# Optimization experiments

Measured on AMD Instinct MI355X. Metric: run time of the kernel, lower is better.

## Reference

```python
import jax, jax.numpy as jnp
import numpy as np

C = 128  # in_channels

def setup_inputs() -> dict:
    key = jax.random.key(0)
    k1, k2, k3, k4 = jax.random.split(key, 4)
    b, c, h, w = 4, C, 64, 64
    feature0 = jax.random.normal(k1, (b, c, h, w), dtype=jnp.float32)
    flow = jax.random.normal(k2, (b, 2, h, w), dtype=jnp.float32)
    # Linear weights stored torch-style as [out, in]; xavier-uniform-like scale
    lim = float(np.sqrt(6.0 / (c + c)))
    Wq = jax.random.uniform(k3, (c, c), minval=-lim, maxval=lim, dtype=jnp.float32)
    Wk = jax.random.uniform(k4, (c, c), minval=-lim, maxval=lim, dtype=jnp.float32)
    bq = jnp.zeros((c,), dtype=jnp.float32)
    bk = jnp.zeros((c,), dtype=jnp.float32)
    return {"feature0": feature0, "flow": flow, "Wq": Wq, "bq": bq, "Wk": Wk, "bk": bk}

def reference(feature0, flow, Wq, bq, Wk, bk):
    b, c, h, w = feature0.shape
    n = h * w
    # [b, n, c]
    x = feature0.reshape(b, c, n).transpose(0, 2, 1)
    query = x @ Wq.T + bq                     # q_proj(feature0)
    key = query @ Wk.T + bk                   # NOTE: k_proj applied to query (as in source)
    value = flow.reshape(b, flow.shape[1], n).transpose(0, 2, 1)  # [b, n, 2]
    scores = jnp.einsum('bnc,bmc->bnm', query, key) / jnp.sqrt(jnp.float32(c))
    prob = jax.nn.softmax(scores, axis=-1)    # [b, n, n]
    out = jnp.einsum('bnm,bmv->bnv', prob, value)  # [b, n, 2]
    return out.reshape(b, h, w, value.shape[-1]).transpose(0, 3, 1, 2)
```

## Files before the change

kernel.cpp:

```cpp
#include <hip/hip_runtime.h>
#include <hip/hip_bf16.h>

constexpr int CH = 128;
constexpr int NPOS = 4096;
constexpr int NB = 4;
constexpr int SPLITS = 8;

typedef __bf16 bf16x8 __attribute__((ext_vector_type(8)));
typedef float f32x2 __attribute__((ext_vector_type(2)));
typedef float f32x16 __attribute__((ext_vector_type(16)));

constexpr float CSC = 0.08838834764831845f * 1.4426950408889634f;


__device__ __forceinline__ void async_copy16(const void* g, void* l) {
  auto gp = (const __attribute__((address_space(1))) unsigned int*)((uintptr_t)g);
  auto lp = (__attribute__((address_space(3))) unsigned int*)((uintptr_t)l);
  __builtin_amdgcn_global_load_lds(gp, lp, 16, 0, 0);
}

#define PIPE_BARRIER(N)                                              \
  asm volatile("s_waitcnt vmcnt(" #N ") lgkmcnt(0)\n\ts_barrier" ::: "memory")

__global__ __launch_bounds__(128) void fuse_w_kernel(
    const float* __restrict__ Wq, const float* __restrict__ bq,
    const float* __restrict__ Wk, const float* __restrict__ bk,
    __bf16* __restrict__ Wqb, __bf16* __restrict__ Wqkb,
    float* __restrict__ bqk) {
  __shared__ float red[CH];
  const int o = blockIdx.x;
  const int i = threadIdx.x;
  float acc = 0.f;
#pragma unroll 8
  for (int m = 0; m < CH; m++) acc += Wk[o * CH + m] * Wq[m * CH + i];
  Wqkb[o * CH + i] = (__bf16)acc;
  Wqb[o * CH + i] = (__bf16)Wq[o * CH + i];
  red[i] = Wk[o * CH + i] * bq[i];
  __syncthreads();
  if (i == 0) {
    float s = 0.f;
    for (int m = 0; m < CH; m++) s += red[m];
    bqk[o] = s + bk[o];
  }
}

__global__ __launch_bounds__(64) void proj_kernel(
    const float* __restrict__ feature0, const __bf16* __restrict__ Wqb,
    const float* __restrict__ bq, const __bf16* __restrict__ Wqkb,
    const float* __restrict__ bqk, __bf16* __restrict__ Qf,
    __bf16* __restrict__ Kf) {
  const int bid = blockIdx.x;
  const int b = (bid >> 1) & 3;
  const int u = (bid >> 3) * 2 + (bid & 1);
  const int lane = threadIdx.x;
  const int half = lane >> 5, l31 = lane & 31;
  const int pos = u * 32 + l31;

  bf16x8 A[8];
#pragma unroll
  for (int ks = 0; ks < 8; ks++) {
    float v[8];
#pragma unroll
    for (int j = 0; j < 8; j++)
      v[j] = feature0[(size_t)(b * CH + ks * 16 + half * 8 + j) * NPOS + pos];
#pragma unroll
    for (int j = 0; j < 8; j++) A[ks][j] = (__bf16)v[j];
  }

#pragma unroll
  for (int z = 0; z < 2; z++) {
    const __bf16* W = z ? Wqkb : Wqb;
    const float* bias = z ? bqk : bq;
    __bf16* Out = z ? Kf : Qf;
    const float scale = z ? 1.0f : CSC;
#pragma unroll
    for (int n = 0; n < 4; n++) {
      const int co = n * 32 + l31;
      const bf16x8* Bp = (const bf16x8*)(W + co * CH + half * 8);
      f32x16 c = {0.f, 0.f, 0.f, 0.f, 0.f, 0.f, 0.f, 0.f,
                  0.f, 0.f, 0.f, 0.f, 0.f, 0.f, 0.f, 0.f};
#pragma unroll
      for (int ks = 0; ks < 8; ks++)
        c = __builtin_amdgcn_mfma_f32_32x32x16_bf16(A[ks], Bp[ks * 2], c, 0, 0,
                                                    0);
      const float bv = bias[co];
      const int kf = n * 2 + (l31 >> 4);
      const int lanebit = (l31 >> 3) & 1;
      const int j = l31 & 7;
#pragma unroll
      for (int r = 0; r < 16; r++) {
        int roff = (r & 3) + 8 * (r >> 2) + 4 * half;
        Out[((((size_t)(b * (NPOS / 32) + u)) * 8 + kf) * 64 +
             (roff + 32 * lanebit)) * 8 + j] = (__bf16)((c[r] + bv) * scale);
      }
    }
  }
}

__global__ __launch_bounds__(256, 4) void attn_kernel(
    const __bf16* __restrict__ Qf, const __bf16* __restrict__ Kf,
    const float* __restrict__ flow, float* __restrict__ part) {
  __shared__ __bf16 Klds[3][8 * 512];
  __shared__ float flds[2 * 512];
  __shared__ float red[128 * 3];

  const int bid = blockIdx.x;
  const int b = (bid >> 1) & 3;
  const int u = (bid >> 3) * 2 + (bid & 1);
  const int split = u >> 5;
  const int qg = u & 31;

  const int tid = threadIdx.x;
  const int wave = tid >> 6, lane = tid & 63;
  const int half = lane >> 5, l31 = lane & 31;
  const int kbase = split * (NPOS / SPLITS);
  constexpr int NT = NPOS / SPLITS / 32;

  {
    const float* fl0 = flow + (size_t)(b * 2 + 0) * NPOS + kbase;
    const float* fl1 = flow + (size_t)(b * 2 + 1) * NPOS + kbase;
    for (int i = tid; i < 512; i += 256) {
      flds[i] = fl0[i];
      flds[512 + i] = fl1[i];
    }
  }

  const int qt = qg * 4 + wave;
  bf16x8 qf[8];
  {
    const bf16x8* Qp =
        (const bf16x8*)Qf + ((size_t)(b * (NPOS / 32) + qt) * 8) * 64 + lane;
#pragma unroll
    for (int kf = 0; kf < 8; kf++) qf[kf] = Qp[kf * 64];
  }

  const __bf16* Ktb =
      Kf + ((size_t)(b * (NPOS / 32) + (kbase >> 5)) * 8) * 512;

  auto issue = [&](int t, int buf) {
    const __bf16* g = Ktb + (size_t)t * (8 * 512);
#pragma unroll
    for (int cc = 0; cc < 2; cc++) {
      int chunk = wave * 2 + cc;
      async_copy16(g + chunk * 512 + lane * 8,
                   &Klds[buf][chunk * 512 + lane * 8]);
    }
  };
  issue(0, 0);
  issue(1, 1);

  float ls[16];
  f32x2 av[16];
#pragma unroll
  for (int r = 0; r < 16; r++) {
    ls[r] = 0.f;
    av[r] = f32x2{0.f, 0.f};
  }

  int bcur = 0, bnext = 2;
  for (int t = 0; t < NT; t++) {
    PIPE_BARRIER(2);
    if (t + 2 < NT) issue(t + 2, bnext);

    const __bf16* kb = &Klds[bcur][0];
    f32x16 c = {0.f, 0.f, 0.f, 0.f, 0.f, 0.f, 0.f, 0.f,
                0.f, 0.f, 0.f, 0.f, 0.f, 0.f, 0.f, 0.f};
#pragma unroll
    for (int kf = 0; kf < 8; kf++) {
      bf16x8 bfrag = *(const bf16x8*)(kb + kf * 512 + lane * 8);
      c = __builtin_amdgcn_mfma_f32_32x32x16_bf16(qf[kf], bfrag, c, 0, 0, 0);
    }
    const f32x2 v01 = {flds[t * 32 + l31], flds[512 + t * 32 + l31]};
#pragma unroll
    for (int r = 0; r < 16; r++) {
      float p = __builtin_amdgcn_exp2f(c[r]);
      ls[r] += p;
      av[r] += f32x2{p, p} * v01;
    }
    bcur = (bcur == 2) ? 0 : bcur + 1;
    bnext = (bnext == 2) ? 0 : bnext + 1;
  }

#pragma unroll
  for (int r = 0; r < 16; r++) {
#pragma unroll
    for (int st = 1; st < 32; st <<= 1) {
      ls[r] += __shfl_xor(ls[r], st, 64);
      av[r][0] += __shfl_xor(av[r][0], st, 64);
      av[r][1] += __shfl_xor(av[r][1], st, 64);
    }
  }
  if (l31 == 0) {
#pragma unroll
    for (int r = 0; r < 16; r++) {
      int ql = wave * 32 + (r & 3) + 8 * (r >> 2) + 4 * half;
      red[ql * 3 + 0] = ls[r];
      red[ql * 3 + 1] = av[r][0];
      red[ql * 3 + 2] = av[r][1];
    }
  }
  __syncthreads();
  for (int idx = tid; idx < 128 * 3; idx += 256) {
    int plane = idx / 128, ql = idx % 128;
    part[((size_t)(plane * SPLITS + split) * NB + b) * NPOS + qg * 128 + ql] =
        red[ql * 3 + plane];
  }
}

__global__ __launch_bounds__(256) void combine_kernel(
    const float* __restrict__ part, float* __restrict__ out) {
  int t = blockIdx.x * 256 + threadIdx.x;
  int b = t >> 12, q = t & (NPOS - 1);
  float l = 0.f, x = 0.f, y = 0.f;
#pragma unroll
  for (int s = 0; s < SPLITS; s++) {
    l += part[((size_t)(0 * SPLITS + s) * NB + b) * NPOS + q];
    x += part[((size_t)(1 * SPLITS + s) * NB + b) * NPOS + q];
    y += part[((size_t)(2 * SPLITS + s) * NB + b) * NPOS + q];
  }
  float inv = 1.0f / l;
  out[(size_t)(b * 2 + 0) * NPOS + q] = x * inv;
  out[(size_t)(b * 2 + 1) * NPOS + q] = y * inv;
}

extern "C" void kernel_launch(void* const* d_in, const int* in_sizes, int n_in,
                              void* d_out, int out_size, void* d_ws,
                              size_t ws_size, hipStream_t stream) {
  const float* feature0 = (const float*)d_in[0];
  const float* flow = (const float*)d_in[1];
  const float* Wq = (const float*)d_in[2];
  const float* bq = (const float*)d_in[3];
  const float* Wk = (const float*)d_in[4];
  const float* bk = (const float*)d_in[5];
  float* out = (float*)d_out;

  char* ws = (char*)d_ws;
  __bf16* Qf = (__bf16*)ws;
  __bf16* Kf = (__bf16*)(ws + (4 << 20));
  __bf16* Wqb = (__bf16*)(ws + (8 << 20));
  __bf16* Wqkb = (__bf16*)(ws + (8 << 20) + (32 << 10));
  float* bqk = (float*)(ws + (8 << 20) + (64 << 10));
  float* part = (float*)(ws + (8 << 20) + (128 << 10));

  fuse_w_kernel<<<dim3(CH), 128, 0, stream>>>(Wq, bq, Wk, bk, Wqb, Wqkb, bqk);
  proj_kernel<<<dim3(512), 64, 0, stream>>>(feature0, Wqb, bq, Wqkb, bqk, Qf,
                                            Kf);
  attn_kernel<<<dim3(1024), 256, 0, stream>>>(Qf, Kf, flow, part);
  combine_kernel<<<dim3(NB * NPOS / 256), 256, 0, stream>>>(part, out);
}
```

Baseline: 114.3 us.

## Replace async LDS loads with register-staged double buffering; split projection grid

The attention kernel stops using direct global-to-LDS async copies with a triple buffer. It now stages K tiles through registers into a double buffer holding two 32-key subtiles per step, and runs two independent MFMA chains per iteration. The occupancy hint drops from 4 to 3 blocks per CU. The projection kernel launches twice as many blocks, each computing only Q or only K, which trades redundant feature loads for more parallelism. The register staging adds VGPR pressure and moves the barrier wait to lgkmcnt only, so global loads are exposed differently.

```diff
diff --git a/kernel.cpp b/kernel.cpp
--- a/kernel.cpp
+++ b/kernel.cpp
@@ -13,14 +13,8 @@
 constexpr float CSC = 0.08838834764831845f * 1.4426950408889634f;
 
 
-__device__ __forceinline__ void async_copy16(const void* g, void* l) {
-  auto gp = (const __attribute__((address_space(1))) unsigned int*)((uintptr_t)g);
-  auto lp = (__attribute__((address_space(3))) unsigned int*)((uintptr_t)l);
-  __builtin_amdgcn_global_load_lds(gp, lp, 16, 0, 0);
-}
-
-#define PIPE_BARRIER(N)                                              \
-  asm volatile("s_waitcnt vmcnt(" #N ") lgkmcnt(0)\n\ts_barrier" ::: "memory")
+#define LGKM_BARRIER() \
+  asm volatile("s_waitcnt lgkmcnt(0)\n\ts_barrier" ::: "memory")
 
 __global__ __launch_bounds__(128) void fuse_w_kernel(
     const float* __restrict__ Wq, const float* __restrict__ bq,
@@ -51,7 +45,8 @@
     __bf16* __restrict__ Kf) {
   const int bid = blockIdx.x;
   const int b = (bid >> 1) & 3;
-  const int u = (bid >> 3) * 2 + (bid & 1);
+  const int uz = (bid >> 3) * 2 + (bid & 1);
+  const int u = uz >> 1, z = uz & 1;
   const int lane = threadIdx.x;
   const int half = lane >> 5, l31 = lane & 31;
   const int pos = u * 32 + l31;
@@ -67,40 +62,37 @@
     for (int j = 0; j < 8; j++) A[ks][j] = (__bf16)v[j];
   }
 
-#pragma unroll
-  for (int z = 0; z < 2; z++) {
-    const __bf16* W = z ? Wqkb : Wqb;
-    const float* bias = z ? bqk : bq;
-    __bf16* Out = z ? Kf : Qf;
-    const float scale = z ? 1.0f : CSC;
-#pragma unroll
-    for (int n = 0; n < 4; n++) {
-      const int co = n * 32 + l31;
-      const bf16x8* Bp = (const bf16x8*)(W + co * CH + half * 8);
-      f32x16 c = {0.f, 0.f, 0.f, 0.f, 0.f, 0.f, 0.f, 0.f,
-                  0.f, 0.f, 0.f, 0.f, 0.f, 0.f, 0.f, 0.f};
-#pragma unroll
-      for (int ks = 0; ks < 8; ks++)
-        c = __builtin_amdgcn_mfma_f32_32x32x16_bf16(A[ks], Bp[ks * 2], c, 0, 0,
-                                                    0);
-      const float bv = bias[co];
-      const int kf = n * 2 + (l31 >> 4);
-      const int lanebit = (l31 >> 3) & 1;
-      const int j = l31 & 7;
-#pragma unroll
-      for (int r = 0; r < 16; r++) {
-        int roff = (r & 3) + 8 * (r >> 2) + 4 * half;
-        Out[((((size_t)(b * (NPOS / 32) + u)) * 8 + kf) * 64 +
-             (roff + 32 * lanebit)) * 8 + j] = (__bf16)((c[r] + bv) * scale);
-      }
-    }
-  }
-}
-
-__global__ __launch_bounds__(256, 4) void attn_kernel(
+  const __bf16* W = z ? Wqkb : Wqb;
+  const float* bias = z ? bqk : bq;
+  __bf16* Out = z ? Kf : Qf;
+  const float scale = z ? 1.0f : CSC;
+#pragma unroll
+  for (int n = 0; n < 4; n++) {
+    const int co = n * 32 + l31;
+    const bf16x8* Bp = (const bf16x8*)(W + co * CH + half * 8);
+    f32x16 c = {0.f, 0.f, 0.f, 0.f, 0.f, 0.f, 0.f, 0.f,
+                0.f, 0.f, 0.f, 0.f, 0.f, 0.f, 0.f, 0.f};
+#pragma unroll
+    for (int ks = 0; ks < 8; ks++)
+      c = __builtin_amdgcn_mfma_f32_32x32x16_bf16(A[ks], Bp[ks * 2], c, 0, 0,
+                                                  0);
+    const float bv = bias[co];
+    const int kf = n * 2 + (l31 >> 4);
+    const int lanebit = (l31 >> 3) & 1;
+    const int j = l31 & 7;
+#pragma unroll
+    for (int r = 0; r < 16; r++) {
+      int roff = (r & 3) + 8 * (r >> 2) + 4 * half;
+      Out[((((size_t)(b * (NPOS / 32) + u)) * 8 + kf) * 64 +
+           (roff + 32 * lanebit)) * 8 + j] = (__bf16)((c[r] + bv) * scale);
+    }
+  }
+}
+
+__global__ __launch_bounds__(256, 3) void attn_kernel(
     const __bf16* __restrict__ Qf, const __bf16* __restrict__ Kf,
     const float* __restrict__ flow, float* __restrict__ part) {
-  __shared__ __bf16 Klds[3][8 * 512];
+  __shared__ __bf16 Klds[2][8192];
   __shared__ float flds[2 * 512];
   __shared__ float red[128 * 3];
 
@@ -114,7 +106,24 @@
   const int wave = tid >> 6, lane = tid & 63;
   const int half = lane >> 5, l31 = lane & 31;
   const int kbase = split * (NPOS / SPLITS);
-  constexpr int NT = NPOS / SPLITS / 32;
+  constexpr int NT = 8;
+
+  const __bf16* Ktb =
+      Kf + ((size_t)(b * (NPOS / 32) + (kbase >> 5))) * 4096;
+
+  uint4 g[4];
+  auto load_tile = [&](int t) {
+    const uint4* gp = (const uint4*)(Ktb + (size_t)t * 8192);
+#pragma unroll
+    for (int i = 0; i < 4; i++) g[i] = gp[tid + i * 256];
+  };
+  auto write_tile = [&](int buf) {
+    uint4* lp = (uint4*)&Klds[buf][0];
+#pragma unroll
+    for (int i = 0; i < 4; i++) lp[tid + i * 256] = g[i];
+  };
+
+  load_tile(0);
 
   {
     const float* fl0 = flow + (size_t)(b * 2 + 0) * NPOS + kbase;
@@ -134,20 +143,8 @@
     for (int kf = 0; kf < 8; kf++) qf[kf] = Qp[kf * 64];
   }
 
-  const __bf16* Ktb =
-      Kf + ((size_t)(b * (NPOS / 32) + (kbase >> 5)) * 8) * 512;
-
-  auto issue = [&](int t, int buf) {
-    const __bf16* g = Ktb + (size_t)t * (8 * 512);
-#pragma unroll
-    for (int cc = 0; cc < 2; cc++) {
-      int chunk = wave * 2 + cc;
-      async_copy16(g + chunk * 512 + lane * 8,
-                   &Klds[buf][chunk * 512 + lane * 8]);
-    }
-  };
-  issue(0, 0);
-  issue(1, 1);
+  write_tile(0);
+  load_tile(1);
 
   float ls[16];
   f32x2 av[16];
@@ -157,28 +154,37 @@
     av[r] = f32x2{0.f, 0.f};
   }
 
-  int bcur = 0, bnext = 2;
   for (int t = 0; t < NT; t++) {
-    PIPE_BARRIER(2);
-    if (t + 2 < NT) issue(t + 2, bnext);
-
-    const __bf16* kb = &Klds[bcur][0];
-    f32x16 c = {0.f, 0.f, 0.f, 0.f, 0.f, 0.f, 0.f, 0.f,
-                0.f, 0.f, 0.f, 0.f, 0.f, 0.f, 0.f, 0.f};
+    LGKM_BARRIER();
+    if (t + 1 < NT) {
+      write_tile((t + 1) & 1);
+      if (t + 2 < NT) load_tile(t + 2);
+    }
+
+    const __bf16* kb = &Klds[t & 1][0];
+    f32x16 cA = {0.f, 0.f, 0.f, 0.f, 0.f, 0.f, 0.f, 0.f,
+                 0.f, 0.f, 0.f, 0.f, 0.f, 0.f, 0.f, 0.f};
+    f32x16 cB = cA;
 #pragma unroll
     for (int kf = 0; kf < 8; kf++) {
-      bf16x8 bfrag = *(const bf16x8*)(kb + kf * 512 + lane * 8);
-      c = __builtin_amdgcn_mfma_f32_32x32x16_bf16(qf[kf], bfrag, c, 0, 0, 0);
-    }
-    const f32x2 v01 = {flds[t * 32 + l31], flds[512 + t * 32 + l31]};
+      bf16x8 fA = *(const bf16x8*)(kb + kf * 512 + lane * 8);
+      cA = __builtin_amdgcn_mfma_f32_32x32x16_bf16(qf[kf], fA, cA, 0, 0, 0);
+    }
+#pragma unroll
+    for (int kf = 0; kf < 8; kf++) {
+      bf16x8 fB = *(const bf16x8*)(kb + 4096 + kf * 512 + lane * 8);
+      cB = __builtin_amdgcn_mfma_f32_32x32x16_bf16(qf[kf], fB, cB, 0, 0, 0);
+    }
+
+    const f32x2 vA = {flds[t * 64 + l31], flds[512 + t * 64 + l31]};
+    const f32x2 vB = {flds[t * 64 + 32 + l31], flds[512 + t * 64 + 32 + l31]};
 #pragma unroll
     for (int r = 0; r < 16; r++) {
-      float p = __builtin_amdgcn_exp2f(c[r]);
-      ls[r] += p;
-      av[r] += f32x2{p, p} * v01;
-    }
-    bcur = (bcur == 2) ? 0 : bcur + 1;
-    bnext = (bnext == 2) ? 0 : bnext + 1;
+      float pA = __builtin_amdgcn_exp2f(cA[r]);
+      float pB = __builtin_amdgcn_exp2f(cB[r]);
+      ls[r] += pA + pB;
+      av[r] += f32x2{pA, pA} * vA + f32x2{pB, pB} * vB;
+    }
   }
 
 #pragma unroll
@@ -243,8 +249,8 @@
   float* part = (float*)(ws + (8 << 20) + (128 << 10));
 
   fuse_w_kernel<<<dim3(CH), 128, 0, stream>>>(Wq, bq, Wk, bk, Wqb, Wqkb, bqk);
-  proj_kernel<<<dim3(512), 64, 0, stream>>>(feature0, Wqb, bq, Wqkb, bqk, Qf,
-                                            Kf);
+  proj_kernel<<<dim3(1024), 64, 0, stream>>>(feature0, Wqb, bq, Wqkb, bqk, Qf,
+                                             Kf);
   attn_kernel<<<dim3(1024), 256, 0, stream>>>(Qf, Kf, flow, part);
   combine_kernel<<<dim3(NB * NPOS / 256), 256, 0, stream>>>(part, out);
 }
```

Result: slower. 129.4 us (+13.2%).

## Add producer wave for K loads, double key splits, parallelize projection over channels

Applied to the files above, without the earlier changes.

The attention kernel now uses a dedicated fifth wave to issue async global-to-LDS copies of K tiles, while four consumer waves only compute and synchronize through barriers. Key splits double, so each block handles fewer key tiles and the grid doubles. The projection kernel also spreads output-channel tiles and Q/K selection across 4 waves and twice as many blocks instead of looping in one wave. The aim is more parallelism and better overlap of loads with MFMA work. The cost is more partial results for the combine step, redundant feature loads in the projection, and an extra idle-ish wave per block.

```diff
diff --git a/kernel.cpp b/kernel.cpp
--- a/kernel.cpp
+++ b/kernel.cpp
@@ -4,7 +4,7 @@
 constexpr int CH = 128;
 constexpr int NPOS = 4096;
 constexpr int NB = 4;
-constexpr int SPLITS = 8;
+constexpr int SPLITS = 16;
 
 typedef __bf16 bf16x8 __attribute__((ext_vector_type(8)));
 typedef float f32x2 __attribute__((ext_vector_type(2)));
@@ -18,9 +18,6 @@
   auto lp = (__attribute__((address_space(3))) unsigned int*)((uintptr_t)l);
   __builtin_amdgcn_global_load_lds(gp, lp, 16, 0, 0);
 }
-
-#define PIPE_BARRIER(N)                                              \
-  asm volatile("s_waitcnt vmcnt(" #N ") lgkmcnt(0)\n\ts_barrier" ::: "memory")
 
 __global__ __launch_bounds__(128) void fuse_w_kernel(
     const float* __restrict__ Wq, const float* __restrict__ bq,
@@ -44,15 +41,17 @@
   }
 }
 
-__global__ __launch_bounds__(64) void proj_kernel(
+__global__ __launch_bounds__(256) void proj_kernel(
     const float* __restrict__ feature0, const __bf16* __restrict__ Wqb,
     const float* __restrict__ bq, const __bf16* __restrict__ Wqkb,
     const float* __restrict__ bqk, __bf16* __restrict__ Qf,
     __bf16* __restrict__ Kf) {
   const int bid = blockIdx.x;
   const int b = (bid >> 1) & 3;
-  const int u = (bid >> 3) * 2 + (bid & 1);
-  const int lane = threadIdx.x;
+  const int rest = (bid >> 3) * 2 + (bid & 1);
+  const int u = rest >> 1, z = rest & 1;
+  const int n = threadIdx.x >> 6;
+  const int lane = threadIdx.x & 63;
   const int half = lane >> 5, l31 = lane & 31;
   const int pos = u * 32 + l31;
 
@@ -67,41 +66,40 @@
     for (int j = 0; j < 8; j++) A[ks][j] = (__bf16)v[j];
   }
 
-#pragma unroll
-  for (int z = 0; z < 2; z++) {
-    const __bf16* W = z ? Wqkb : Wqb;
-    const float* bias = z ? bqk : bq;
-    __bf16* Out = z ? Kf : Qf;
-    const float scale = z ? 1.0f : CSC;
-#pragma unroll
-    for (int n = 0; n < 4; n++) {
-      const int co = n * 32 + l31;
-      const bf16x8* Bp = (const bf16x8*)(W + co * CH + half * 8);
-      f32x16 c = {0.f, 0.f, 0.f, 0.f, 0.f, 0.f, 0.f, 0.f,
-                  0.f, 0.f, 0.f, 0.f, 0.f, 0.f, 0.f, 0.f};
-#pragma unroll
-      for (int ks = 0; ks < 8; ks++)
-        c = __builtin_amdgcn_mfma_f32_32x32x16_bf16(A[ks], Bp[ks * 2], c, 0, 0,
-                                                    0);
-      const float bv = bias[co];
-      const int kf = n * 2 + (l31 >> 4);
-      const int lanebit = (l31 >> 3) & 1;
-      const int j = l31 & 7;
-#pragma unroll
-      for (int r = 0; r < 16; r++) {
-        int roff = (r & 3) + 8 * (r >> 2) + 4 * half;
-        Out[((((size_t)(b * (NPOS / 32) + u)) * 8 + kf) * 64 +
-             (roff + 32 * lanebit)) * 8 + j] = (__bf16)((c[r] + bv) * scale);
-      }
-    }
-  }
-}
-
-__global__ __launch_bounds__(256, 4) void attn_kernel(
+  const __bf16* W = z ? Wqkb : Wqb;
+  const float* bias = z ? bqk : bq;
+  __bf16* Out = z ? Kf : Qf;
+  const float scale = z ? 1.0f : CSC;
+
+  const int co = n * 32 + l31;
+  const bf16x8* Bp = (const bf16x8*)(W + co * CH + half * 8);
+  f32x16 c = {0.f, 0.f, 0.f, 0.f, 0.f, 0.f, 0.f, 0.f,
+              0.f, 0.f, 0.f, 0.f, 0.f, 0.f, 0.f, 0.f};
+#pragma unroll
+  for (int ks = 0; ks < 8; ks++)
+    c = __builtin_amdgcn_mfma_f32_32x32x16_bf16(A[ks], Bp[ks * 2], c, 0, 0, 0);
+  const float bv = bias[co];
+  const int kf = n * 2 + (l31 >> 4);
+  const int lanebit = (l31 >> 3) & 1;
+  const int j = l31 & 7;
+#pragma unroll
+  for (int r = 0; r < 16; r++) {
+    int roff = (r & 3) + 8 * (r >> 2) + 4 * half;
+    Out[((((size_t)(b * (NPOS / 32) + u)) * 8 + kf) * 64 +
+         (roff + 32 * lanebit)) * 8 + j] = (__bf16)((c[r] + bv) * scale);
+  }
+}
+
+#define CONS_BARRIER() \
+  asm volatile("s_waitcnt vmcnt(0) lgkmcnt(0)\n\ts_barrier" ::: "memory")
+#define PROD_BARRIER(N) \
+  asm volatile("s_waitcnt vmcnt(" #N ")\n\ts_barrier" ::: "memory")
+
+__global__ __launch_bounds__(320, 4) void attn_kernel(
     const __bf16* __restrict__ Qf, const __bf16* __restrict__ Kf,
     const float* __restrict__ flow, float* __restrict__ part) {
-  __shared__ __bf16 Klds[3][8 * 512];
-  __shared__ float flds[2 * 512];
+  __shared__ __bf16 Klds[3][4096];
+  __shared__ float flds[2 * 256];
   __shared__ float red[128 * 3];
 
   const int bid = blockIdx.x;
@@ -113,97 +111,98 @@
   const int tid = threadIdx.x;
   const int wave = tid >> 6, lane = tid & 63;
   const int half = lane >> 5, l31 = lane & 31;
-  const int kbase = split * (NPOS / SPLITS);
-  constexpr int NT = NPOS / SPLITS / 32;
-
-  {
-    const float* fl0 = flow + (size_t)(b * 2 + 0) * NPOS + kbase;
-    const float* fl1 = flow + (size_t)(b * 2 + 1) * NPOS + kbase;
-    for (int i = tid; i < 512; i += 256) {
-      flds[i] = fl0[i];
-      flds[512 + i] = fl1[i];
-    }
-  }
-
-  const int qt = qg * 4 + wave;
-  bf16x8 qf[8];
-  {
-    const bf16x8* Qp =
-        (const bf16x8*)Qf + ((size_t)(b * (NPOS / 32) + qt) * 8) * 64 + lane;
-#pragma unroll
-    for (int kf = 0; kf < 8; kf++) qf[kf] = Qp[kf * 64];
-  }
-
-  const __bf16* Ktb =
-      Kf + ((size_t)(b * (NPOS / 32) + (kbase >> 5)) * 8) * 512;
-
-  auto issue = [&](int t, int buf) {
-    const __bf16* g = Ktb + (size_t)t * (8 * 512);
-#pragma unroll
-    for (int cc = 0; cc < 2; cc++) {
-      int chunk = wave * 2 + cc;
-      async_copy16(g + chunk * 512 + lane * 8,
-                   &Klds[buf][chunk * 512 + lane * 8]);
-    }
-  };
-  issue(0, 0);
-  issue(1, 1);
-
-  float ls[16];
-  f32x2 av[16];
-#pragma unroll
-  for (int r = 0; r < 16; r++) {
-    ls[r] = 0.f;
-    av[r] = f32x2{0.f, 0.f};
-  }
-
-  int bcur = 0, bnext = 2;
-  for (int t = 0; t < NT; t++) {
-    PIPE_BARRIER(2);
-    if (t + 2 < NT) issue(t + 2, bnext);
-
-    const __bf16* kb = &Klds[bcur][0];
-    f32x16 c = {0.f, 0.f, 0.f, 0.f, 0.f, 0.f, 0.f, 0.f,
-                0.f, 0.f, 0.f, 0.f, 0.f, 0.f, 0.f, 0.f};
-#pragma unroll
-    for (int kf = 0; kf < 8; kf++) {
-      bf16x8 bfrag = *(const bf16x8*)(kb + kf * 512 + lane * 8);
-      c = __builtin_amdgcn_mfma_f32_32x32x16_bf16(qf[kf], bfrag, c, 0, 0, 0);
-    }
-    const f32x2 v01 = {flds[t * 32 + l31], flds[512 + t * 32 + l31]};
+  constexpr int NT = 8;
+
+  const __bf16* Ktb = Kf + ((size_t)(b * (NPOS / 32) + split * 8)) * 4096;
+
+  if (wave == 4) {
+    auto issue = [&](int t) {
+      const __bf16* g = Ktb + (size_t)t * 4096;
+      __bf16* l = &Klds[t % 3][0];
+#pragma unroll
+      for (int i = 0; i < 8; i++)
+        async_copy16(g + i * 512 + lane * 8, l + i * 512 + lane * 8);
+    };
+    issue(0);
+    issue(1);
+    PROD_BARRIER(8);
+    for (int t = 0; t < NT; t++) {
+      if (t + 2 < NT) {
+        issue(t + 2);
+        PROD_BARRIER(8);
+      } else {
+        PROD_BARRIER(0);
+      }
+    }
+    asm volatile("s_barrier" ::: "memory");
+  } else {
+    {
+      const float* fl0 = flow + (size_t)(b * 2 + 0) * NPOS + split * 256;
+      const float* fl1 = flow + (size_t)(b * 2 + 1) * NPOS + split * 256;
+      flds[tid] = fl0[tid];
+      flds[256 + tid] = fl1[tid];
+    }
+    const int qt = qg * 4 + wave;
+    bf16x8 qf[8];
+    {
+      const bf16x8* Qp =
+          (const bf16x8*)Qf + ((size_t)(b * (NPOS / 32) + qt) * 8) * 64 + lane;
+#pragma unroll
+      for (int kf = 0; kf < 8; kf++) qf[kf] = Qp[kf * 64];
+    }
+    float ls[16];
+    f32x2 av[16];
 #pragma unroll
     for (int r = 0; r < 16; r++) {
-      float p = __builtin_amdgcn_exp2f(c[r]);
-      ls[r] += p;
-      av[r] += f32x2{p, p} * v01;
-    }
-    bcur = (bcur == 2) ? 0 : bcur + 1;
-    bnext = (bnext == 2) ? 0 : bnext + 1;
-  }
-
-#pragma unroll
-  for (int r = 0; r < 16; r++) {
-#pragma unroll
-    for (int st = 1; st < 32; st <<= 1) {
-      ls[r] += __shfl_xor(ls[r], st, 64);
-      av[r][0] += __shfl_xor(av[r][0], st, 64);
-      av[r][1] += __shfl_xor(av[r][1], st, 64);
-    }
-  }
-  if (l31 == 0) {
+      ls[r] = 0.f;
+      av[r] = f32x2{0.f, 0.f};
+    }
+
+    CONS_BARRIER();
+
+    for (int t = 0; t < NT; t++) {
+      const __bf16* kb = &Klds[t % 3][0];
+      f32x16 c = {0.f, 0.f, 0.f, 0.f, 0.f, 0.f, 0.f, 0.f,
+                  0.f, 0.f, 0.f, 0.f, 0.f, 0.f, 0.f, 0.f};
+#pragma unroll
+      for (int kf = 0; kf < 8; kf++) {
+        bf16x8 bfrag = *(const bf16x8*)(kb + kf * 512 + lane * 8);
+        c = __builtin_amdgcn_mfma_f32_32x32x16_bf16(qf[kf], bfrag, c, 0, 0, 0);
+      }
+      const f32x2 v01 = {flds[t * 32 + l31], flds[256 + t * 32 + l31]};
+#pragma unroll
+      for (int r = 0; r < 16; r++) {
+        float p = __builtin_amdgcn_exp2f(c[r]);
+        ls[r] += p;
+        av[r] += f32x2{p, p} * v01;
+      }
+      CONS_BARRIER();
+    }
+
 #pragma unroll
     for (int r = 0; r < 16; r++) {
-      int ql = wave * 32 + (r & 3) + 8 * (r >> 2) + 4 * half;
-      red[ql * 3 + 0] = ls[r];
-      red[ql * 3 + 1] = av[r][0];
-      red[ql * 3 + 2] = av[r][1];
-    }
-  }
-  __syncthreads();
-  for (int idx = tid; idx < 128 * 3; idx += 256) {
-    int plane = idx / 128, ql = idx % 128;
-    part[((size_t)(plane * SPLITS + split) * NB + b) * NPOS + qg * 128 + ql] =
-        red[ql * 3 + plane];
+#pragma unroll
+      for (int st = 1; st < 32; st <<= 1) {
+        ls[r] += __shfl_xor(ls[r], st, 64);
+        av[r][0] += __shfl_xor(av[r][0], st, 64);
+        av[r][1] += __shfl_xor(av[r][1], st, 64);
+      }
+    }
+    if (l31 == 0) {
+#pragma unroll
+      for (int r = 0; r < 16; r++) {
+        int ql = wave * 32 + (r & 3) + 8 * (r >> 2) + 4 * half;
+        red[ql * 3 + 0] = ls[r];
+        red[ql * 3 + 1] = av[r][0];
+        red[ql * 3 + 2] = av[r][1];
+      }
+    }
+    CONS_BARRIER();
+    for (int idx = tid; idx < 128 * 3; idx += 256) {
+      int plane = idx / 128, ql = idx % 128;
+      part[((size_t)(plane * SPLITS + split) * NB + b) * NPOS + qg * 128 +
+           ql] = red[ql * 3 + plane];
+    }
   }
 }
 
@@ -243,8 +242,8 @@
   float* part = (float*)(ws + (8 << 20) + (128 << 10));
 
   fuse_w_kernel<<<dim3(CH), 128, 0, stream>>>(Wq, bq, Wk, bk, Wqb, Wqkb, bqk);
-  proj_kernel<<<dim3(512), 64, 0, stream>>>(feature0, Wqb, bq, Wqkb, bqk, Qf,
-                                            Kf);
-  attn_kernel<<<dim3(1024), 256, 0, stream>>>(Qf, Kf, flow, part);
+  proj_kernel<<<dim3(1024), 256, 0, stream>>>(feature0, Wqb, bq, Wqkb, bqk, Qf,
+                                              Kf);
+  attn_kernel<<<dim3(2048), 320, 0, stream>>>(Qf, Kf, flow, part);
   combine_kernel<<<dim3(NB * NPOS / 256), 256, 0, stream>>>(part, out);
 }
```

Measured after the change: 135.8 us. 18.8% more time.
